# Kernel tuning notes

Hardware: AMD Instinct MI355X
Metric: run time of the kernel (lower is better)

The kernel has to match this reference:

```python
import jax, jax.numpy as jnp
import numpy as np

B, C, H, W = 2, 48, 64, 64
EPS = 1e-5
ROW = [0, 0, 0, H // 4, H // 4, H // 4, H // 2, H // 2, H // 2]
COL = [0, W // 4, W // 2] * 3


def setup_inputs() -> dict:
    key = jax.random.key(0)
    ks = iter(jax.random.split(key, 40))
    s = 1.0 / np.sqrt(C)  # keep unscaled-softmax logits sane
    def rn(shape, scale=1.0):
        return jax.random.normal(next(ks), shape, jnp.float32) * scale
    def ru(shape):
        return jax.random.uniform(next(ks), shape, jnp.float32, 0.5, 1.5)
    return dict(
        input_feature=rn((B, C, H, W)), feat_b=rn((B, C, H, W)),
        feat_c=rn((B, C, H, W)), feat_d=rn((B, C, H, W)),
        W_fa_all=rn((C, C), s), W_fb_all=rn((C, C), s),
        W_fc_all=rn((C, C), s), W_fd_all=rn((C, C), s),
        W_fa=rn((9, C, C), s), W_fb=rn((9, C, C), s),
        W_fc=rn((9, C, C), s), W_fd=rn((9, C, C), s),
        fuse_w=rn((C, 4 * C), s), fuse_b=rn((C,), 0.1),
        fuse_g=ru((C,)), fuse_bb=rn((C,), 0.1), fuse_m=rn((C,), 0.1), fuse_v=ru((C,)),
        fuseP_w=rn((9, C, 4 * C), s), fuseP_b=rn((9, C), 0.1),
        fuseP_g=ru((9, C)), fuseP_bb=rn((9, C), 0.1), fuseP_m=rn((9, C), 0.1), fuseP_v=ru((9, C)),
        gamma_all=rn(()), gamma_p=rn((9,)),
        out_w=rn((C, C, 3, 3), s / 3.0), out_b=rn((C,), 0.1),
        out_g=ru((C,)), out_bb=rn((C,), 0.1), out_m=rn((C,), 0.1), out_v=ru((C,)),
    )


def _attn(q, k, v):
    # q,k,v: [..., C, N] -> energy [..., N, N]; non-standard softmax(max - energy)
    e = jnp.einsum('...cn,...cm->...nm', q, k)
    e = jnp.max(e, axis=-1, keepdims=True) - e
    a = jax.nn.softmax(e, axis=-1)
    return jnp.einsum('...cn,...nm->...cm', v, a)  # torch.matmul(v, attention)


def reference(input_feature, feat_b, feat_c, feat_d,
              W_fa_all, W_fb_all, W_fc_all, W_fd_all,
              W_fa, W_fb, W_fc, W_fd,
              fuse_w, fuse_b, fuse_g, fuse_bb, fuse_m, fuse_v,
              fuseP_w, fuseP_b, fuseP_g, fuseP_bb, fuseP_m, fuseP_v,
              gamma_all, gamma_p,
              out_w, out_b, out_g, out_bb, out_m, out_v):
    h2, w2 = H // 2, W // 2
    N = H * W
    # ---- global branch: channel-wise Linear (bias=False) applied over spatial tokens
    fa = jnp.einsum('dc,bcn->bdn', W_fa_all, input_feature.reshape(B, C, N))
    fb = jnp.einsum('dc,bcn->bdn', W_fb_all, feat_b.reshape(B, C, N))
    fc = jnp.einsum('dc,bcn->bdn', W_fc_all, feat_c.reshape(B, C, N))
    fd = jnp.einsum('dc,bcn->bdn', W_fd_all, feat_d.reshape(B, C, N))
    cat = jnp.concatenate([_attn(fa, fa, fa), _attn(fa, fb, fb),
                           _attn(fa, fc, fc), _attn(fa, fd, fd)], axis=1)
    cat = cat.reshape(B, 4 * C, H, W)
    y = jnp.einsum('oc,bchw->bohw', fuse_w, cat) + fuse_b[None, :, None, None]
    y = (y - fuse_m[:, None, None]) * (fuse_g / jnp.sqrt(fuse_v + EPS))[:, None, None] + fuse_bb[:, None, None]
    atten_all = jax.nn.relu(y)  # Dropout2d is identity at eval
    # ---- 9 overlapping patch branches, vectorized over the patch axis p
    def crops(x):
        return jnp.stack([x[:, :, r:r + h2, c:c + w2] for r, c in zip(ROW, COL)], 0).reshape(9, B, C, h2 * w2)
    pa = jnp.einsum('pdc,pbcn->pbdn', W_fa, crops(input_feature))
    pb = jnp.einsum('pdc,pbcn->pbdn', W_fb, crops(feat_b))
    pc = jnp.einsum('pdc,pbcn->pbdn', W_fc, crops(feat_c))
    pd = jnp.einsum('pdc,pbcn->pbdn', W_fd, crops(feat_d))
    pcat = jnp.concatenate([_attn(pa, pa, pa), _attn(pa, pb, pb),
                            _attn(pa, pc, pc), _attn(pa, pd, pd)], axis=2)
    pcat = pcat.reshape(9, B, 4 * C, h2, w2)
    py = jnp.einsum('poc,pbchw->pbohw', fuseP_w, pcat) + fuseP_b[:, None, :, None, None]
    py = ((py - fuseP_m[:, None, :, None, None])
          * (fuseP_g / jnp.sqrt(fuseP_v + EPS))[:, None, :, None, None]
          + fuseP_bb[:, None, :, None, None])
    patch_out = 0.5 * gamma_p[:, None, None, None, None] * jax.nn.relu(py)
    # ---- combine (overlapping patch regions accumulate additively, as in torch +=)
    out = input_feature + gamma_all * atten_all
    for i, (r, c) in enumerate(zip(ROW, COL)):
        out = out.at[:, :, r:r + h2, c:c + w2].add(patch_out[i])
    # ---- to_out: 3x3 conv + BN(eval) + ReLU
    z = jax.lax.conv_general_dilated(out, out_w, (1, 1), 'SAME',
                                     dimension_numbers=('NCHW', 'OIHW', 'NCHW'))
    z = z + out_b[None, :, None, None]
    z = (z - out_m[:, None, None]) * (out_g / jnp.sqrt(out_v + EPS))[:, None, None] + out_bb[:, None, None]
    return jax.nn.relu(z)
```

## Files before the change

### kernel.cpp

```cpp
#include <hip/hip_runtime.h>
#include <math.h>

typedef _Float16 f16;
typedef f16 f16x8 __attribute__((ext_vector_type(8)));
typedef float f32x4 __attribute__((ext_vector_type(4)));

namespace {
constexpr int B_ = 2, C_ = 48, H_ = 64, W_ = 64;
constexpr int N_ = H_ * W_;
constexpr int NP_ = 1024;
constexpr int C4_ = 4 * C_;
constexpr float EPS_ = 1e-5f;
constexpr float L2E_ = 1.44269504f;
constexpr float REFL2_ = -25.0f * 1.44269504f;
}

#define MFMA32(a, b, c) __builtin_amdgcn_mfma_f32_16x16x32_f16((a), (b), (c), 0, 0, 0)

__device__ inline float fast_exp2(float x) {
#if __has_builtin(__builtin_amdgcn_exp2f)
  return __builtin_amdgcn_exp2f(x);
#else
  float r;
  asm("v_exp_f32 %0, %1" : "=v"(r) : "v"(x));
  return r;
#endif
}

__global__ __launch_bounds__(256) void k_proj_g(
    const float* __restrict__ x0, const float* __restrict__ x1,
    const float* __restrict__ x2, const float* __restrict__ x3,
    const float* __restrict__ w0, const float* __restrict__ w1,
    const float* __restrict__ w2, const float* __restrict__ w3,
    f16* __restrict__ pn, f16* __restrict__ pt) {
  __shared__ float Ws[48 * 48];
  int tid = threadIdx.x;
  int b = blockIdx.y, X = blockIdx.z;
  const float* xp = X == 0 ? x0 : X == 1 ? x1 : X == 2 ? x2 : x3;
  const float* wp = X == 0 ? w0 : X == 1 ? w1 : X == 2 ? w2 : w3;
  for (int i = tid; i < 2304; i += 256) Ws[i] = wp[i];
  __syncthreads();
  int n = blockIdx.x * 256 + tid;
  const float* xb = xp + (size_t)b * 48 * 4096 + n;
  float acc[48];
#pragma unroll
  for (int d = 0; d < 48; ++d) acc[d] = 0.f;
  for (int c0 = 0; c0 < 48; c0 += 4) {
    float xv0 = xb[(size_t)(c0 + 0) * 4096];
    float xv1 = xb[(size_t)(c0 + 1) * 4096];
    float xv2 = xb[(size_t)(c0 + 2) * 4096];
    float xv3 = xb[(size_t)(c0 + 3) * 4096];
#pragma unroll
    for (int d = 0; d < 48; ++d) {
      const float4 wv = *(const float4*)&Ws[d * 48 + c0];
      acc[d] = fmaf(wv.x, xv0, fmaf(wv.y, xv1, fmaf(wv.z, xv2, fmaf(wv.w, xv3, acc[d]))));
    }
  }
  int z2 = X * 2 + b;
  f16* pnb = pn + ((size_t)z2 * 48) * 4096 + n;
#pragma unroll
  for (int d = 0; d < 48; ++d) pnb[(size_t)d * 4096] = (f16)acc[d];
  f16* ptb = pt + ((size_t)z2 * 4096 + n) * 64;
#pragma unroll
  for (int s = 0; s < 6; ++s) {
    f16x8 v;
#pragma unroll
    for (int j = 0; j < 8; ++j) v[j] = (f16)acc[s * 8 + j];
    *(f16x8*)(ptb + s * 8) = v;
  }
  f16x8 zv = {0, 0, 0, 0, 0, 0, 0, 0};
  *(f16x8*)(ptb + 48) = zv;
  *(f16x8*)(ptb + 56) = zv;
}

__global__ __launch_bounds__(256) void k_proj_p(
    const float* __restrict__ x0, const float* __restrict__ x1,
    const float* __restrict__ x2, const float* __restrict__ x3,
    const float* __restrict__ w0, const float* __restrict__ w1,
    const float* __restrict__ w2, const float* __restrict__ w3,
    f16* __restrict__ pn, f16* __restrict__ pt) {
  __shared__ float Ws[48 * 48];
  int tid = threadIdx.x;
  int p = blockIdx.y;
  int X = blockIdx.z >> 1, b = blockIdx.z & 1;
  const float* xp = X == 0 ? x0 : X == 1 ? x1 : X == 2 ? x2 : x3;
  const float* wp = (X == 0 ? w0 : X == 1 ? w1 : X == 2 ? w2 : w3) + (size_t)p * 2304;
  for (int i = tid; i < 2304; i += 256) Ws[i] = wp[i];
  __syncthreads();
  int t = blockIdx.x * 256 + tid;
  int r0 = (p / 3) * 16, c0w = (p % 3) * 16;
  int rr = r0 + (t >> 5), cc = c0w + (t & 31);
  const float* xb = xp + (size_t)b * 48 * 4096 + rr * 64 + cc;
  float acc[48];
#pragma unroll
  for (int d = 0; d < 48; ++d) acc[d] = 0.f;
  for (int c0 = 0; c0 < 48; c0 += 4) {
    float xv0 = xb[(size_t)(c0 + 0) * 4096];
    float xv1 = xb[(size_t)(c0 + 1) * 4096];
    float xv2 = xb[(size_t)(c0 + 2) * 4096];
    float xv3 = xb[(size_t)(c0 + 3) * 4096];
#pragma unroll
    for (int d = 0; d < 48; ++d) {
      const float4 wv = *(const float4*)&Ws[d * 48 + c0];
      acc[d] = fmaf(wv.x, xv0, fmaf(wv.y, xv1, fmaf(wv.z, xv2, fmaf(wv.w, xv3, acc[d]))));
    }
  }
  int z9 = (X * 2 + b) * 9 + p;
  f16* pnb = pn + ((size_t)z9 * 48) * 1024 + t;
#pragma unroll
  for (int d = 0; d < 48; ++d) pnb[(size_t)d * 1024] = (f16)acc[d];
  f16* ptb = pt + ((size_t)z9 * 1024 + t) * 64;
#pragma unroll
  for (int s = 0; s < 6; ++s) {
    f16x8 v;
#pragma unroll
    for (int j = 0; j < 8; ++j) v[j] = (f16)acc[s * 8 + j];
    *(f16x8*)(ptb + s * 8) = v;
  }
  f16x8 zv = {0, 0, 0, 0, 0, 0, 0, 0};
  *(f16x8*)(ptb + 48) = zv;
  *(f16x8*)(ptb + 56) = zv;
}

template <int NT, int NSPLIT, bool PATCH>
__device__ __attribute__((always_inline)) void stats_body(
    const f16* __restrict__ qT_all, const f16* __restrict__ kT_all,
    float* __restrict__ stp, int bx, int by, uint4* Ks) {
  constexpr int MTI = (NT / NSPLIT) / 64;
  int tid = threadIdx.x, wave = tid >> 6, lane = tid & 63, g = lane >> 4, lm = lane & 15;
  int ms = by % NSPLIT, z = by / NSPLIT;
  const f16* qT;
  if (PATCH) {
    int b = (z / 9) % 2, p = z % 9;
    qT = qT_all + ((size_t)(b * 9 + p)) * NT * 64;
  } else {
    int b = z & 1;
    qT = qT_all + (size_t)b * NT * 64;
  }
  const f16* kT = kT_all + (size_t)z * NT * 64;
  int n0 = bx * 128 + wave * 16;
  f16x8 aq0a = *(const f16x8*)(qT + (size_t)(n0 + lm) * 64 + g * 8);
  f16x8 aq1a = *(const f16x8*)(qT + (size_t)(n0 + lm) * 64 + 32 + g * 8);
  f16x8 aq0b = *(const f16x8*)(qT + (size_t)(n0 + 64 + lm) * 64 + g * 8);
  f16x8 aq1b = *(const f16x8*)(qT + (size_t)(n0 + 64 + lm) * 64 + 32 + g * 8);
  const int s0r = tid >> 3, s0c = (tid & 7) * 8;
  const int sw0 = tid ^ ((tid >> 3) & 7);
  const int sw1 = (tid + 256) ^ (((tid + 256) >> 3) & 7);
  const int swl = lm & 7;
  const int c0i = g ^ swl, c1i = (4 + g) ^ swl;
  int t_beg = ms * MTI;
  {
    const f16* src = kT + (size_t)t_beg * 64 * 64;
    Ks[sw0] = *(const uint4*)(src + (size_t)s0r * 64 + s0c);
    Ks[sw1] = *(const uint4*)(src + (size_t)(s0r + 32) * 64 + s0c);
  }
  __syncthreads();
  float zsa[4] = {0.f, 0.f, 0.f, 0.f};
  float zsb[4] = {0.f, 0.f, 0.f, 0.f};
  for (int mt = 0; mt < MTI; ++mt) {
    int cur = mt & 1;
    bool pf = (mt + 1 < MTI);
    uint4 k0v, k1v;
    if (pf) {
      const f16* src = kT + (size_t)(t_beg + mt + 1) * 64 * 64;
      k0v = *(const uint4*)(src + (size_t)s0r * 64 + s0c);
      k1v = *(const uint4*)(src + (size_t)(s0r + 32) * 64 + s0c);
    }
    uint4* kb = Ks + cur * 512;
#pragma unroll
    for (int mf = 0; mf < 4; ++mf) {
      f16x8 b0 = __builtin_bit_cast(f16x8, kb[(16 * mf + lm) * 8 + c0i]);
      f16x8 b1 = __builtin_bit_cast(f16x8, kb[(16 * mf + lm) * 8 + c1i]);
      f32x4 ea = {0.f, 0.f, 0.f, 0.f};
      ea = MFMA32(aq0a, b0, ea);
      ea = MFMA32(aq1a, b1, ea);
      f32x4 eb = {0.f, 0.f, 0.f, 0.f};
      eb = MFMA32(aq0b, b0, eb);
      eb = MFMA32(aq1b, b1, eb);
#pragma unroll
      for (int r = 0; r < 4; ++r) {
        zsa[r] += fast_exp2(fmaf(ea[r], -L2E_, REFL2_));
        zsb[r] += fast_exp2(fmaf(eb[r], -L2E_, REFL2_));
      }
    }
    if (pf) {
      uint4* kn = Ks + (cur ^ 1) * 512;
      kn[sw0] = k0v;
      kn[sw1] = k1v;
    }
    __syncthreads();
  }
#pragma unroll
  for (int mask = 1; mask < 16; mask <<= 1) {
#pragma unroll
    for (int r = 0; r < 4; ++r) {
      zsa[r] += __shfl_xor(zsa[r], mask, 64);
      zsb[r] += __shfl_xor(zsb[r], mask, 64);
    }
  }
  if (lm == 0) {
#pragma unroll
    for (int r = 0; r < 4; ++r) {
      stp[((size_t)z * NT + n0 + 4 * g + r) * NSPLIT + ms] = zsa[r];
      stp[((size_t)z * NT + n0 + 64 + 4 * g + r) * NSPLIT + ms] = zsb[r];
    }
  }
}

__global__ __launch_bounds__(256, 4) void k_stats_all(
    const f16* __restrict__ pg_t, float* __restrict__ stpg,
    const f16* __restrict__ pp_t, float* __restrict__ stpp) {
  __shared__ uint4 Ks[2 * 512];
  int bid = blockIdx.x;
  if (bid < 1024) {
    stats_body<N_, 4, false>(pg_t, pg_t, stpg, bid & 31, bid >> 5, Ks);
  } else {
    int pid = bid - 1024;
    stats_body<NP_, 1, true>(pp_t, pp_t, stpp, pid & 7, pid >> 3, Ks);
  }
}

__global__ __launch_bounds__(256) void k_merge_all(
    const float* __restrict__ stpg, float* __restrict__ stg,
    const float* __restrict__ stpp, float* __restrict__ stp2) {
  int i = blockIdx.x * 256 + threadIdx.x;
  if (i < 8 * N_) {
    const float* p = stpg + (size_t)i * 4;
    float Z = p[0] + p[1] + p[2] + p[3];
    stg[i] = REFL2_ - __log2f(Z);
  } else {
    int j = i - 8 * N_;
    if (j < 72 * NP_) stp2[j] = REFL2_ - __log2f(stpp[j]);
  }
}

template <int NT, int NSPLIT, bool PATCH>
__device__ __attribute__((always_inline)) void pv_body(
    const f16* __restrict__ qT_all, const f16* __restrict__ kT_all,
    const f16* __restrict__ vN_all, const float* __restrict__ st_all,
    float* __restrict__ out_all, int bx, int by,
    float* As2, uint4* Qs, uint4* Vs, uint2* wt2) {
  constexpr int CH = NT / NSPLIT;
  constexpr int NTI = CH / 64;
  int tid = threadIdx.x, wave = tid >> 6, lane = tid & 63, g = lane >> 4, lm = lane & 15;
  int ns = by % NSPLIT, z = by / NSPLIT;
  const f16 *qT, *kT, *vN;
  float* op;
  if (PATCH) {
    int X = z / 18, b = (z / 9) % 2, p = z % 9;
    qT = qT_all + ((size_t)(b * 9 + p)) * NT * 64;
    op = out_all + ((size_t)((p * 2 + b) * C4_ + X * 48)) * NT;
  } else {
    int X = z >> 1, b = z & 1;
    qT = qT_all + (size_t)b * NT * 64;
    op = out_all + ((size_t)(b * C4_ + X * 48)) * NT;
  }
  kT = kT_all + (size_t)z * NT * 64;
  vN = vN_all + (size_t)z * 48 * NT;
  const float* st = st_all + (size_t)z * NT + ns * CH;
  ((float4*)As2)[tid] = ((const float4*)st)[tid];
  int mwa = bx * 128 + wave * 16;
  int mwb = mwa + 64;
  f16x8 bk0a = *(const f16x8*)(kT + (size_t)(mwa + lm) * 64 + g * 8);
  f16x8 bk1a = *(const f16x8*)(kT + (size_t)(mwa + lm) * 64 + 32 + g * 8);
  f16x8 bk0b = *(const f16x8*)(kT + (size_t)(mwb + lm) * 64 + g * 8);
  f16x8 bk1b = *(const f16x8*)(kT + (size_t)(mwb + lm) * 64 + 32 + g * 8);
  const int s0r = tid >> 3, s0c = (tid & 7) * 8;
  const int sw0 = tid ^ ((tid >> 3) & 7);
  const int sw1 = (tid + 256) ^ (((tid + 256) >> 3) & 7);
  const int swl = lm & 7;
  const int c0i = g ^ swl, c1i = (4 + g) ^ swl;
  int t_beg = ns * NTI;
  {
    const f16* qsrc = qT + (size_t)t_beg * 64 * 64;
    Qs[sw0] = *(const uint4*)(qsrc + (size_t)s0r * 64 + s0c);
    Qs[sw1] = *(const uint4*)(qsrc + (size_t)(s0r + 32) * 64 + s0c);
    Vs[sw0] = *(const uint4*)(vN + (size_t)s0r * NT + t_beg * 64 + s0c);
    if (tid < 128)
      Vs[sw1] = *(const uint4*)(vN + (size_t)(s0r + 32) * NT + t_beg * 64 + s0c);
  }
  __syncthreads();
  f32x4 oa0 = {0.f, 0.f, 0.f, 0.f}, oa1 = {0.f, 0.f, 0.f, 0.f}, oa2 = {0.f, 0.f, 0.f, 0.f};
  f32x4 ob0 = {0.f, 0.f, 0.f, 0.f}, ob1 = {0.f, 0.f, 0.f, 0.f}, ob2 = {0.f, 0.f, 0.f, 0.f};
  int wbufa = wave * 512;
  int wbufb = wave * 512 + 256;
  int rba = wbufa + lm * 16;
  int rbb = wbufb + lm * 16;
  for (int nt = 0; nt < NTI; ++nt) {
    bool pf = (nt + 1 < NTI);
    uint4 q0v, q1v, v0v, v1v;
    if (pf) {
      int tn = t_beg + nt + 1;
      const f16* qsrc = qT + (size_t)tn * 64 * 64;
      q0v = *(const uint4*)(qsrc + (size_t)s0r * 64 + s0c);
      q1v = *(const uint4*)(qsrc + (size_t)(s0r + 32) * 64 + s0c);
      v0v = *(const uint4*)(vN + (size_t)s0r * NT + tn * 64 + s0c);
      if (tid < 128)
        v1v = *(const uint4*)(vN + (size_t)(s0r + 32) * NT + tn * 64 + s0c);
    }
    f32x4 ea[4], eb[4];
#pragma unroll
    for (int nf = 0; nf < 4; ++nf) {
      f16x8 a0 = __builtin_bit_cast(f16x8, Qs[(16 * nf + lm) * 8 + c0i]);
      f16x8 a1 = __builtin_bit_cast(f16x8, Qs[(16 * nf + lm) * 8 + c1i]);
      f32x4 ta = {0.f, 0.f, 0.f, 0.f};
      ta = MFMA32(a0, bk0a, ta);
      ta = MFMA32(a1, bk1a, ta);
      ea[nf] = ta;
      f32x4 tb = {0.f, 0.f, 0.f, 0.f};
      tb = MFMA32(a0, bk0b, tb);
      tb = MFMA32(a1, bk1b, tb);
      eb[nf] = tb;
    }
#pragma unroll
    for (int nf = 0; nf < 4; ++nf) {
      float4 a4 = *(const float4*)&As2[nt * 64 + nf * 16 + g * 4];
      float wa0 = fast_exp2(fmaf(ea[nf][0], -L2E_, a4.x));
      float wa1 = fast_exp2(fmaf(ea[nf][1], -L2E_, a4.y));
      float wa2 = fast_exp2(fmaf(ea[nf][2], -L2E_, a4.z));
      float wa3 = fast_exp2(fmaf(ea[nf][3], -L2E_, a4.w));
      float wb0 = fast_exp2(fmaf(eb[nf][0], -L2E_, a4.x));
      float wb1 = fast_exp2(fmaf(eb[nf][1], -L2E_, a4.y));
      float wb2 = fast_exp2(fmaf(eb[nf][2], -L2E_, a4.z));
      float wb3 = fast_exp2(fmaf(eb[nf][3], -L2E_, a4.w));
      unsigned la = __builtin_bit_cast(unsigned, __builtin_amdgcn_cvt_pkrtz(wa0, wa1));
      unsigned ha = __builtin_bit_cast(unsigned, __builtin_amdgcn_cvt_pkrtz(wa2, wa3));
      unsigned lb = __builtin_bit_cast(unsigned, __builtin_amdgcn_cvt_pkrtz(wb0, wb1));
      unsigned hb = __builtin_bit_cast(unsigned, __builtin_amdgcn_cvt_pkrtz(wb2, wb3));
      int s = 2 * nf + (g >> 1);
      int so = ((s ^ swl) * 2) + (g & 1);
      wt2[wbufa + lm * 16 + so] = make_uint2(la, ha);
      wt2[wbufb + lm * 16 + so] = make_uint2(lb, hb);
    }
    __builtin_amdgcn_sched_barrier(0);
    f16x8 bw0a = __builtin_bit_cast(f16x8, *(const uint4*)&wt2[rba + c0i * 2]);
    f16x8 bw1a = __builtin_bit_cast(f16x8, *(const uint4*)&wt2[rba + c1i * 2]);
    f16x8 bw0b = __builtin_bit_cast(f16x8, *(const uint4*)&wt2[rbb + c0i * 2]);
    f16x8 bw1b = __builtin_bit_cast(f16x8, *(const uint4*)&wt2[rbb + c1i * 2]);
#pragma unroll
    for (int cf = 0; cf < 3; ++cf) {
      f16x8 av0 = __builtin_bit_cast(f16x8, Vs[(16 * cf + lm) * 8 + c0i]);
      f16x8 av1 = __builtin_bit_cast(f16x8, Vs[(16 * cf + lm) * 8 + c1i]);
      if (cf == 0) {
        oa0 = MFMA32(av0, bw0a, oa0); oa0 = MFMA32(av1, bw1a, oa0);
        ob0 = MFMA32(av0, bw0b, ob0); ob0 = MFMA32(av1, bw1b, ob0);
      }
      if (cf == 1) {
        oa1 = MFMA32(av0, bw0a, oa1); oa1 = MFMA32(av1, bw1a, oa1);
        ob1 = MFMA32(av0, bw0b, ob1); ob1 = MFMA32(av1, bw1b, ob1);
      }
      if (cf == 2) {
        oa2 = MFMA32(av0, bw0a, oa2); oa2 = MFMA32(av1, bw1a, oa2);
        ob2 = MFMA32(av0, bw0b, ob2); ob2 = MFMA32(av1, bw1b, ob2);
      }
    }
    __syncthreads();
    if (pf) {
      Qs[sw0] = q0v;
      Qs[sw1] = q1v;
      Vs[sw0] = v0v;
      if (tid < 128) Vs[sw1] = v1v;
    }
    __syncthreads();
  }
  if (NSPLIT == 1) {
#pragma unroll
    for (int r = 0; r < 4; ++r) {
      op[(size_t)(0 + 4 * g + r) * NT + mwa + lm] = oa0[r];
      op[(size_t)(16 + 4 * g + r) * NT + mwa + lm] = oa1[r];
      op[(size_t)(32 + 4 * g + r) * NT + mwa + lm] = oa2[r];
      op[(size_t)(0 + 4 * g + r) * NT + mwb + lm] = ob0[r];
      op[(size_t)(16 + 4 * g + r) * NT + mwb + lm] = ob1[r];
      op[(size_t)(32 + 4 * g + r) * NT + mwb + lm] = ob2[r];
    }
  } else {
#pragma unroll
    for (int r = 0; r < 4; ++r) {
      atomicAdd(&op[(size_t)(0 + 4 * g + r) * NT + mwa + lm], oa0[r]);
      atomicAdd(&op[(size_t)(16 + 4 * g + r) * NT + mwa + lm], oa1[r]);
      atomicAdd(&op[(size_t)(32 + 4 * g + r) * NT + mwa + lm], oa2[r]);
      atomicAdd(&op[(size_t)(0 + 4 * g + r) * NT + mwb + lm], ob0[r]);
      atomicAdd(&op[(size_t)(16 + 4 * g + r) * NT + mwb + lm], ob1[r]);
      atomicAdd(&op[(size_t)(32 + 4 * g + r) * NT + mwb + lm], ob2[r]);
    }
  }
}

__global__ __launch_bounds__(256, 4) void k_pv_all(
    const f16* __restrict__ pg_t, const f16* __restrict__ pg_n,
    const float* __restrict__ statsg, float* __restrict__ cat,
    const f16* __restrict__ pp_t, const f16* __restrict__ pp_n,
    const float* __restrict__ statsp, float* __restrict__ pcat) {
  __shared__ float As2[1024];
  __shared__ uint4 Qs[512];
  __shared__ uint4 Vs[384];
  __shared__ uint2 wt2[2048];
  int bid = blockIdx.x;
  if (bid < 1024) {
    pv_body<N_, 4, false>(pg_t, pg_t, pg_n, statsg, cat, bid & 31, bid >> 5,
                          As2, Qs, Vs, wt2);
  } else {
    int pid = bid - 1024;
    pv_body<NP_, 1, true>(pp_t, pp_t, pp_n, statsp, pcat, pid & 7, pid >> 3,
                          As2, Qs, Vs, wt2);
  }
}

__global__ __launch_bounds__(256) void k_fuse_global(
    const float* __restrict__ cat, const float* __restrict__ fw,
    const float* __restrict__ fb, const float* __restrict__ fg,
    const float* __restrict__ fbb, const float* __restrict__ fm,
    const float* __restrict__ fv, const float* __restrict__ gamma_all,
    const float* __restrict__ input, float* __restrict__ comb) {
  int idx = blockIdx.x * 256 + threadIdx.x;
  int n4 = idx & 1023;
  int rest = idx >> 10;
  int o = rest % C_;
  int b = rest / C_;
  const float* cr = cat + (size_t)b * C4_ * N_ + n4 * 4;
  const float* wr = fw + (size_t)o * C4_;
  float4 acc = {0.f, 0.f, 0.f, 0.f};
#pragma unroll 8
  for (int c = 0; c < C4_; ++c) {
    float4 xv = *(const float4*)(cr + (size_t)c * N_);
    float w = wr[c];
    acc.x = fmaf(w, xv.x, acc.x); acc.y = fmaf(w, xv.y, acc.y);
    acc.z = fmaf(w, xv.z, acc.z); acc.w = fmaf(w, xv.w, acc.w);
  }
  float scale = fg[o] * rsqrtf(fv[o] + EPS_);
  float sh = fb[o] - fm[o], bb = fbb[o], ga = gamma_all[0];
  float4 inv = *(const float4*)(input + ((size_t)(b * C_ + o) * N_) + n4 * 4);
  float4 out;
  out.x = inv.x + ga * fmaxf((acc.x + sh) * scale + bb, 0.f);
  out.y = inv.y + ga * fmaxf((acc.y + sh) * scale + bb, 0.f);
  out.z = inv.z + ga * fmaxf((acc.z + sh) * scale + bb, 0.f);
  out.w = inv.w + ga * fmaxf((acc.w + sh) * scale + bb, 0.f);
  *(float4*)(comb + ((size_t)(b * C_ + o) * N_) + n4 * 4) = out;
}

__global__ __launch_bounds__(256) void k_fuse_patch(
    const float* __restrict__ pcat, const float* __restrict__ fw,
    const float* __restrict__ fb, const float* __restrict__ fg,
    const float* __restrict__ fbb, const float* __restrict__ fm,
    const float* __restrict__ fv, const float* __restrict__ gamma_p,
    float* __restrict__ py) {
  int idx = blockIdx.x * 256 + threadIdx.x;
  int t4 = idx & 255;
  int rest = idx >> 8;
  int o = rest % C_; rest /= C_;
  int b = rest % B_;
  int p = rest / B_;
  const float* cr = pcat + ((size_t)(p * B_ + b) * C4_) * NP_ + t4 * 4;
  const float* wr = fw + (size_t)(p * C_ + o) * C4_;
  float4 acc = {0.f, 0.f, 0.f, 0.f};
#pragma unroll 8
  for (int c = 0; c < C4_; ++c) {
    float4 xv = *(const float4*)(cr + (size_t)c * NP_);
    float w = wr[c];
    acc.x = fmaf(w, xv.x, acc.x); acc.y = fmaf(w, xv.y, acc.y);
    acc.z = fmaf(w, xv.z, acc.z); acc.w = fmaf(w, xv.w, acc.w);
  }
  int po = p * C_ + o;
  float scale = fg[po] * rsqrtf(fv[po] + EPS_);
  float sh = fb[po] - fm[po], bb = fbb[po], gp = 0.5f * gamma_p[p];
  float4 out;
  out.x = gp * fmaxf((acc.x + sh) * scale + bb, 0.f);
  out.y = gp * fmaxf((acc.y + sh) * scale + bb, 0.f);
  out.z = gp * fmaxf((acc.z + sh) * scale + bb, 0.f);
  out.w = gp * fmaxf((acc.w + sh) * scale + bb, 0.f);
  *(float4*)(py + ((size_t)(p * B_ + b) * C_ + o) * NP_ + t4 * 4) = out;
}

__global__ __launch_bounds__(256) void k_combine(
    const float* __restrict__ py, const float* __restrict__ comb,
    f16* __restrict__ combh) {
  int idx = blockIdx.x * 256 + threadIdx.x;
  int w = idx & (W_ - 1);
  int h = (idx >> 6) & (H_ - 1);
  int rest = idx >> 12;
  int ch = rest % C_;
  int b = rest / C_;
  float val = comb[idx];
#pragma unroll
  for (int p = 0; p < 9; ++p) {
    int r0 = (p / 3) * 16, c0 = (p % 3) * 16;
    if (h >= r0 && h < r0 + 32 && w >= c0 && w < c0 + 32)
      val += py[((size_t)(p * B_ + b) * C_ + ch) * NP_ + (h - r0) * 32 + (w - c0)];
  }
  combh[idx] = (f16)val;
}

__global__ __launch_bounds__(256) void k_conv2(
    const f16* __restrict__ combh, const float* __restrict__ cw,
    const float* __restrict__ cb, const float* __restrict__ cg,
    const float* __restrict__ cbb, const float* __restrict__ cm,
    const float* __restrict__ cv, float* __restrict__ out) {
  __shared__ uint4 inh[2304];
  int tid = threadIdx.x;
  int h0 = blockIdx.x * 4, ocg = blockIdx.y, b = blockIdx.z;
  for (int i = tid; i < 2304; i += 256) {
    int c = i / 48;
    int rem = i - c * 48;
    int r = rem >> 3, u = rem & 7;
    int hh = h0 - 1 + r;
    uint4 val = make_uint4(0, 0, 0, 0);
    if (hh >= 0 && hh < H_)
      val = *(const uint4*)(combh + (((size_t)(b * C_ + c) * H_ + hh) * W_ + u * 8));
    inh[i] = val;
  }
  __syncthreads();
  int w = tid & 63, dh = tid >> 6;
  float acc[6] = {0.f, 0.f, 0.f, 0.f, 0.f, 0.f};
  const f16* lds = (const f16*)inh;
  int wm = w > 0 ? w - 1 : 0;
  int wp = w < 63 ? w + 1 : 63;
  for (int c = 0; c < 48; ++c) {
    float v[9];
#pragma unroll
    for (int r = 0; r < 3; ++r) {
      const f16* row = lds + (size_t)(c * 6 + dh + r) * 64;
      float lf = (float)row[wm];
      float md = (float)row[w];
      float rt = (float)row[wp];
      v[r * 3 + 0] = (w > 0) ? lf : 0.f;
      v[r * 3 + 1] = md;
      v[r * 3 + 2] = (w < 63) ? rt : 0.f;
    }
#pragma unroll
    for (int j = 0; j < 6; ++j) {
      const float* wr = cw + (size_t)((ocg * 6 + j) * 48 + c) * 9;
#pragma unroll
      for (int k = 0; k < 9; ++k) acc[j] = fmaf(v[k], wr[k], acc[j]);
    }
  }
#pragma unroll
  for (int j = 0; j < 6; ++j) {
    int o = ocg * 6 + j;
    float scale = cg[o] * rsqrtf(cv[o] + EPS_);
    float y = (acc[j] + cb[o] - cm[o]) * scale + cbb[o];
    out[(size_t)(b * C_ + o) * N_ + (h0 + dh) * 64 + w] = fmaxf(y, 0.f);
  }
}

extern "C" void kernel_launch(void* const* d_in, const int* in_sizes, int n_in,
                              void* d_out, int out_size, void* d_ws, size_t ws_size,
                              hipStream_t stream) {
  (void)in_sizes; (void)n_in; (void)out_size; (void)ws_size;
  const float* x[4];
  const float* Wall[4];
  const float* Wp[4];
  for (int i = 0; i < 4; ++i) {
    x[i] = (const float*)d_in[i];
    Wall[i] = (const float*)d_in[4 + i];
    Wp[i] = (const float*)d_in[8 + i];
  }
  const float* fuse_w = (const float*)d_in[12];
  const float* fuse_b = (const float*)d_in[13];
  const float* fuse_g = (const float*)d_in[14];
  const float* fuse_bb = (const float*)d_in[15];
  const float* fuse_m = (const float*)d_in[16];
  const float* fuse_v = (const float*)d_in[17];
  const float* fuseP_w = (const float*)d_in[18];
  const float* fuseP_b = (const float*)d_in[19];
  const float* fuseP_g = (const float*)d_in[20];
  const float* fuseP_bb = (const float*)d_in[21];
  const float* fuseP_m = (const float*)d_in[22];
  const float* fuseP_v = (const float*)d_in[23];
  const float* gamma_all = (const float*)d_in[24];
  const float* gamma_p = (const float*)d_in[25];
  const float* out_w = (const float*)d_in[26];
  const float* out_b = (const float*)d_in[27];
  const float* out_g = (const float*)d_in[28];
  const float* out_bb = (const float*)d_in[29];
  const float* out_m = (const float*)d_in[30];
  const float* out_v = (const float*)d_in[31];

  char* base = (char*)d_ws;
  size_t off = 0;
  auto carve = [&](size_t bytes) {
    char* p = base + off;
    off += (bytes + 255) & ~(size_t)255;
    return p;
  };
  f16* projg_n = (f16*)carve((size_t)8 * 48 * N_ * 2);
  f16* projg_t = (f16*)carve((size_t)8 * N_ * 64 * 2);
  f16* projp_n = (f16*)carve((size_t)72 * 48 * NP_ * 2);
  f16* projp_t = (f16*)carve((size_t)72 * NP_ * 64 * 2);
  float* stpg = (float*)carve((size_t)8 * N_ * 4 * 4);
  float* stpp = (float*)carve((size_t)72 * NP_ * 4);
  float* statsg = (float*)carve((size_t)8 * N_ * 4);
  float* statsp = (float*)carve((size_t)72 * NP_ * 4);
  float* cat = (float*)carve((size_t)B_ * C4_ * N_ * 4);
  float* pcat = (float*)carve((size_t)9 * B_ * C4_ * NP_ * 4);
  float* comb = (float*)carve((size_t)B_ * C_ * N_ * 4);
  float* py = (float*)carve((size_t)9 * B_ * C_ * NP_ * 4);
  f16* combh = (f16*)carve((size_t)B_ * C_ * N_ * 2);

  dim3 blk(256);

  k_proj_g<<<dim3(16, 2, 4), blk, 0, stream>>>(
      x[0], x[1], x[2], x[3], Wall[0], Wall[1], Wall[2], Wall[3], projg_n, projg_t);
  k_proj_p<<<dim3(4, 9, 8), blk, 0, stream>>>(
      x[0], x[1], x[2], x[3], Wp[0], Wp[1], Wp[2], Wp[3], projp_n, projp_t);

  k_stats_all<<<dim3(1600), blk, 0, stream>>>(projg_t, stpg, projp_t, stpp);
  k_merge_all<<<dim3((8 * N_ + 72 * NP_ + 255) / 256), blk, 0, stream>>>(
      stpg, statsg, stpp, statsp);

  (void)hipMemsetAsync(cat, 0, (size_t)B_ * C4_ * N_ * sizeof(float), stream);
  k_pv_all<<<dim3(1600), blk, 0, stream>>>(
      projg_t, projg_n, statsg, cat, projp_t, projp_n, statsp, pcat);

  k_fuse_global<<<(B_ * C_ * (N_ / 4)) / 256, blk, 0, stream>>>(
      cat, fuse_w, fuse_b, fuse_g, fuse_bb, fuse_m, fuse_v, gamma_all, x[0], comb);
  k_fuse_patch<<<(9 * B_ * C_ * (NP_ / 4)) / 256, blk, 0, stream>>>(
      pcat, fuseP_w, fuseP_b, fuseP_g, fuseP_bb, fuseP_m, fuseP_v, gamma_p, py);
  k_combine<<<(B_ * C_ * N_) / 256, blk, 0, stream>>>(py, comb, combh);
  k_conv2<<<dim3(16, 8, 2), blk, 0, stream>>>(
      combh, out_w, out_b, out_g, out_bb, out_m, out_v, (float*)d_out);
}
```

Baseline: 262.0 us.

## Merge projection and fuse kernels, drop LDS stats staging, raise stats occupancy

Merges the global and patch projection kernels into one launch, and likewise the global and patch fuse kernels, so fewer kernels launch and the small grids share the GPU. The PV kernel now reads the softmax stats straight from global memory instead of staging them in shared memory, which saves LDS and a store. The stats kernel's launch-bounds occupancy hint goes from 4 to 6 blocks. The memset is moved earlier in the stream. Risks are more register pressure in the stats kernel and extra global loads for the stats reads.

```diff
diff --git a/kernel.cpp b/kernel.cpp
--- a/kernel.cpp
+++ b/kernel.cpp
@@ -27,21 +27,9 @@
 #endif
 }
 
-__global__ __launch_bounds__(256) void k_proj_g(
-    const float* __restrict__ x0, const float* __restrict__ x1,
-    const float* __restrict__ x2, const float* __restrict__ x3,
-    const float* __restrict__ w0, const float* __restrict__ w1,
-    const float* __restrict__ w2, const float* __restrict__ w3,
-    f16* __restrict__ pn, f16* __restrict__ pt) {
-  __shared__ float Ws[48 * 48];
-  int tid = threadIdx.x;
-  int b = blockIdx.y, X = blockIdx.z;
-  const float* xp = X == 0 ? x0 : X == 1 ? x1 : X == 2 ? x2 : x3;
-  const float* wp = X == 0 ? w0 : X == 1 ? w1 : X == 2 ? w2 : w3;
-  for (int i = tid; i < 2304; i += 256) Ws[i] = wp[i];
-  __syncthreads();
-  int n = blockIdx.x * 256 + tid;
-  const float* xb = xp + (size_t)b * 48 * 4096 + n;
+__device__ __attribute__((always_inline)) void proj_body(
+    const float* __restrict__ xb, const float* __restrict__ Ws,
+    f16* __restrict__ pnb, size_t pn_stride, f16* __restrict__ ptb) {
   float acc[48];
 #pragma unroll
   for (int d = 0; d < 48; ++d) acc[d] = 0.f;
@@ -56,11 +44,8 @@
       acc[d] = fmaf(wv.x, xv0, fmaf(wv.y, xv1, fmaf(wv.z, xv2, fmaf(wv.w, xv3, acc[d]))));
     }
   }
-  int z2 = X * 2 + b;
-  f16* pnb = pn + ((size_t)z2 * 48) * 4096 + n;
-#pragma unroll
-  for (int d = 0; d < 48; ++d) pnb[(size_t)d * 4096] = (f16)acc[d];
-  f16* ptb = pt + ((size_t)z2 * 4096 + n) * 64;
+#pragma unroll
+  for (int d = 0; d < 48; ++d) pnb[(size_t)d * pn_stride] = (f16)acc[d];
 #pragma unroll
   for (int s = 0; s < 6; ++s) {
     f16x8 v;
@@ -73,53 +58,48 @@
   *(f16x8*)(ptb + 56) = zv;
 }
 
-__global__ __launch_bounds__(256) void k_proj_p(
+__global__ __launch_bounds__(256) void k_proj_all(
     const float* __restrict__ x0, const float* __restrict__ x1,
     const float* __restrict__ x2, const float* __restrict__ x3,
     const float* __restrict__ w0, const float* __restrict__ w1,
     const float* __restrict__ w2, const float* __restrict__ w3,
-    f16* __restrict__ pn, f16* __restrict__ pt) {
+    const float* __restrict__ wp0, const float* __restrict__ wp1,
+    const float* __restrict__ wp2, const float* __restrict__ wp3,
+    f16* __restrict__ pgn, f16* __restrict__ pgt,
+    f16* __restrict__ ppn, f16* __restrict__ ppt) {
   __shared__ float Ws[48 * 48];
   int tid = threadIdx.x;
-  int p = blockIdx.y;
-  int X = blockIdx.z >> 1, b = blockIdx.z & 1;
-  const float* xp = X == 0 ? x0 : X == 1 ? x1 : X == 2 ? x2 : x3;
-  const float* wp = (X == 0 ? w0 : X == 1 ? w1 : X == 2 ? w2 : w3) + (size_t)p * 2304;
-  for (int i = tid; i < 2304; i += 256) Ws[i] = wp[i];
-  __syncthreads();
-  int t = blockIdx.x * 256 + tid;
-  int r0 = (p / 3) * 16, c0w = (p % 3) * 16;
-  int rr = r0 + (t >> 5), cc = c0w + (t & 31);
-  const float* xb = xp + (size_t)b * 48 * 4096 + rr * 64 + cc;
-  float acc[48];
-#pragma unroll
-  for (int d = 0; d < 48; ++d) acc[d] = 0.f;
-  for (int c0 = 0; c0 < 48; c0 += 4) {
-    float xv0 = xb[(size_t)(c0 + 0) * 4096];
-    float xv1 = xb[(size_t)(c0 + 1) * 4096];
-    float xv2 = xb[(size_t)(c0 + 2) * 4096];
-    float xv3 = xb[(size_t)(c0 + 3) * 4096];
-#pragma unroll
-    for (int d = 0; d < 48; ++d) {
-      const float4 wv = *(const float4*)&Ws[d * 48 + c0];
-      acc[d] = fmaf(wv.x, xv0, fmaf(wv.y, xv1, fmaf(wv.z, xv2, fmaf(wv.w, xv3, acc[d]))));
-    }
-  }
-  int z9 = (X * 2 + b) * 9 + p;
-  f16* pnb = pn + ((size_t)z9 * 48) * 1024 + t;
-#pragma unroll
-  for (int d = 0; d < 48; ++d) pnb[(size_t)d * 1024] = (f16)acc[d];
-  f16* ptb = pt + ((size_t)z9 * 1024 + t) * 64;
-#pragma unroll
-  for (int s = 0; s < 6; ++s) {
-    f16x8 v;
-#pragma unroll
-    for (int j = 0; j < 8; ++j) v[j] = (f16)acc[s * 8 + j];
-    *(f16x8*)(ptb + s * 8) = v;
-  }
-  f16x8 zv = {0, 0, 0, 0, 0, 0, 0, 0};
-  *(f16x8*)(ptb + 48) = zv;
-  *(f16x8*)(ptb + 56) = zv;
+  int bid = blockIdx.x;
+  if (bid < 128) {
+    int bx = bid & 15, b = (bid >> 4) & 1, X = bid >> 5;
+    const float* xp = X == 0 ? x0 : X == 1 ? x1 : X == 2 ? x2 : x3;
+    const float* wp = X == 0 ? w0 : X == 1 ? w1 : X == 2 ? w2 : w3;
+    for (int i = tid; i < 2304; i += 256) Ws[i] = wp[i];
+    __syncthreads();
+    int n = bx * 256 + tid;
+    int z2 = X * 2 + b;
+    proj_body(xp + (size_t)b * 48 * 4096 + n, Ws,
+              pgn + ((size_t)z2 * 48) * 4096 + n, 4096,
+              pgt + ((size_t)z2 * 4096 + n) * 64);
+  } else {
+    int pid = bid - 128;
+    int bx = pid & 3;
+    int rest = pid >> 2;
+    int p = rest % 9;
+    int zb = rest / 9;
+    int X = zb >> 1, b = zb & 1;
+    const float* xp = X == 0 ? x0 : X == 1 ? x1 : X == 2 ? x2 : x3;
+    const float* wp = (X == 0 ? wp0 : X == 1 ? wp1 : X == 2 ? wp2 : wp3) + (size_t)p * 2304;
+    for (int i = tid; i < 2304; i += 256) Ws[i] = wp[i];
+    __syncthreads();
+    int t = bx * 256 + tid;
+    int r0 = (p / 3) * 16, c0w = (p % 3) * 16;
+    int rr = r0 + (t >> 5), cc = c0w + (t & 31);
+    int z9 = (X * 2 + b) * 9 + p;
+    proj_body(xp + (size_t)b * 48 * 4096 + rr * 64 + cc, Ws,
+              ppn + ((size_t)z9 * 48) * 1024 + t, 1024,
+              ppt + ((size_t)z9 * 1024 + t) * 64);
+  }
 }
 
 template <int NT, int NSPLIT, bool PATCH>
@@ -207,7 +187,7 @@
   }
 }
 
-__global__ __launch_bounds__(256, 4) void k_stats_all(
+__global__ __launch_bounds__(256, 6) void k_stats_all(
     const f16* __restrict__ pg_t, float* __restrict__ stpg,
     const f16* __restrict__ pp_t, float* __restrict__ stpp) {
   __shared__ uint4 Ks[2 * 512];
@@ -239,7 +219,7 @@
     const f16* __restrict__ qT_all, const f16* __restrict__ kT_all,
     const f16* __restrict__ vN_all, const float* __restrict__ st_all,
     float* __restrict__ out_all, int bx, int by,
-    float* As2, uint4* Qs, uint4* Vs, uint2* wt2) {
+    uint4* Qs, uint4* Vs, uint2* wt2) {
   constexpr int CH = NT / NSPLIT;
   constexpr int NTI = CH / 64;
   int tid = threadIdx.x, wave = tid >> 6, lane = tid & 63, g = lane >> 4, lm = lane & 15;
@@ -258,7 +238,6 @@
   kT = kT_all + (size_t)z * NT * 64;
   vN = vN_all + (size_t)z * 48 * NT;
   const float* st = st_all + (size_t)z * NT + ns * CH;
-  ((float4*)As2)[tid] = ((const float4*)st)[tid];
   int mwa = bx * 128 + wave * 16;
   int mwb = mwa + 64;
   f16x8 bk0a = *(const f16x8*)(kT + (size_t)(mwa + lm) * 64 + g * 8);
@@ -314,7 +293,7 @@
     }
 #pragma unroll
     for (int nf = 0; nf < 4; ++nf) {
-      float4 a4 = *(const float4*)&As2[nt * 64 + nf * 16 + g * 4];
+      float4 a4 = *(const float4*)(st + nt * 64 + nf * 16 + g * 4);
       float wa0 = fast_exp2(fmaf(ea[nf][0], -L2E_, a4.x));
       float wa1 = fast_exp2(fmaf(ea[nf][1], -L2E_, a4.y));
       float wa2 = fast_exp2(fmaf(ea[nf][2], -L2E_, a4.z));
@@ -391,84 +370,84 @@
     const float* __restrict__ statsg, float* __restrict__ cat,
     const f16* __restrict__ pp_t, const f16* __restrict__ pp_n,
     const float* __restrict__ statsp, float* __restrict__ pcat) {
-  __shared__ float As2[1024];
   __shared__ uint4 Qs[512];
   __shared__ uint4 Vs[384];
   __shared__ uint2 wt2[2048];
   int bid = blockIdx.x;
   if (bid < 1024) {
     pv_body<N_, 4, false>(pg_t, pg_t, pg_n, statsg, cat, bid & 31, bid >> 5,
-                          As2, Qs, Vs, wt2);
+                          Qs, Vs, wt2);
   } else {
     int pid = bid - 1024;
     pv_body<NP_, 1, true>(pp_t, pp_t, pp_n, statsp, pcat, pid & 7, pid >> 3,
-                          As2, Qs, Vs, wt2);
-  }
-}
-
-__global__ __launch_bounds__(256) void k_fuse_global(
+                          Qs, Vs, wt2);
+  }
+}
+
+__global__ __launch_bounds__(256) void k_fuse_all(
     const float* __restrict__ cat, const float* __restrict__ fw,
     const float* __restrict__ fb, const float* __restrict__ fg,
     const float* __restrict__ fbb, const float* __restrict__ fm,
     const float* __restrict__ fv, const float* __restrict__ gamma_all,
-    const float* __restrict__ input, float* __restrict__ comb) {
-  int idx = blockIdx.x * 256 + threadIdx.x;
-  int n4 = idx & 1023;
-  int rest = idx >> 10;
-  int o = rest % C_;
-  int b = rest / C_;
-  const float* cr = cat + (size_t)b * C4_ * N_ + n4 * 4;
-  const float* wr = fw + (size_t)o * C4_;
-  float4 acc = {0.f, 0.f, 0.f, 0.f};
+    const float* __restrict__ input, float* __restrict__ comb,
+    const float* __restrict__ pcat, const float* __restrict__ pfw,
+    const float* __restrict__ pfb, const float* __restrict__ pfg,
+    const float* __restrict__ pfbb, const float* __restrict__ pfm,
+    const float* __restrict__ pfv, const float* __restrict__ gamma_p,
+    float* __restrict__ py) {
+  int bid = blockIdx.x;
+  if (bid < 384) {
+    int idx = bid * 256 + threadIdx.x;
+    int n4 = idx & 1023;
+    int rest = idx >> 10;
+    int o = rest % C_;
+    int b = rest / C_;
+    const float* cr = cat + (size_t)b * C4_ * N_ + n4 * 4;
+    const float* wr = fw + (size_t)o * C4_;
+    float4 acc = {0.f, 0.f, 0.f, 0.f};
 #pragma unroll 8
-  for (int c = 0; c < C4_; ++c) {
-    float4 xv = *(const float4*)(cr + (size_t)c * N_);
-    float w = wr[c];
-    acc.x = fmaf(w, xv.x, acc.x); acc.y = fmaf(w, xv.y, acc.y);
-    acc.z = fmaf(w, xv.z, acc.z); acc.w = fmaf(w, xv.w, acc.w);
-  }
-  float scale = fg[o] * rsqrtf(fv[o] + EPS_);
-  float sh = fb[o] - fm[o], bb = fbb[o], ga = gamma_all[0];
-  float4 inv = *(const float4*)(input + ((size_t)(b * C_ + o) * N_) + n4 * 4);
-  float4 out;
-  out.x = inv.x + ga * fmaxf((acc.x + sh) * scale + bb, 0.f);
-  out.y = inv.y + ga * fmaxf((acc.y + sh) * scale + bb, 0.f);
-  out.z = inv.z + ga * fmaxf((acc.z + sh) * scale + bb, 0.f);
-  out.w = inv.w + ga * fmaxf((acc.w + sh) * scale + bb, 0.f);
-  *(float4*)(comb + ((size_t)(b * C_ + o) * N_) + n4 * 4) = out;
-}
-
-__global__ __launch_bounds__(256) void k_fuse_patch(
-    const float* __restrict__ pcat, const float* __restrict__ fw,
-    const float* __restrict__ fb, const float* __restrict__ fg,
-    const float* __restrict__ fbb, const float* __restrict__ fm,
-    const float* __restrict__ fv, const float* __restrict__ gamma_p,
-    float* __restrict__ py) {
-  int idx = blockIdx.x * 256 + threadIdx.x;
-  int t4 = idx & 255;
-  int rest = idx >> 8;
-  int o = rest % C_; rest /= C_;
-  int b = rest % B_;
-  int p = rest / B_;
-  const float* cr = pcat + ((size_t)(p * B_ + b) * C4_) * NP_ + t4 * 4;
-  const float* wr = fw + (size_t)(p * C_ + o) * C4_;
-  float4 acc = {0.f, 0.f, 0.f, 0.f};
+    for (int c = 0; c < C4_; ++c) {
+      float4 xv = *(const float4*)(cr + (size_t)c * N_);
+      float w = wr[c];
+      acc.x = fmaf(w, xv.x, acc.x); acc.y = fmaf(w, xv.y, acc.y);
+      acc.z = fmaf(w, xv.z, acc.z); acc.w = fmaf(w, xv.w, acc.w);
+    }
+    float scale = fg[o] * rsqrtf(fv[o] + EPS_);
+    float sh = fb[o] - fm[o], bb = fbb[o], ga = gamma_all[0];
+    float4 inv = *(const float4*)(input + ((size_t)(b * C_ + o) * N_) + n4 * 4);
+    float4 out;
+    out.x = inv.x + ga * fmaxf((acc.x + sh) * scale + bb, 0.f);
+    out.y = inv.y + ga * fmaxf((acc.y + sh) * scale + bb, 0.f);
+    out.z = inv.z + ga * fmaxf((acc.z + sh) * scale + bb, 0.f);
+    out.w = inv.w + ga * fmaxf((acc.w + sh) * scale + bb, 0.f);
+    *(float4*)(comb + ((size_t)(b * C_ + o) * N_) + n4 * 4) = out;
+  } else {
+    int idx = (bid - 384) * 256 + threadIdx.x;
+    int t4 = idx & 255;
+    int rest = idx >> 8;
+    int o = rest % C_; rest /= C_;
+    int b = rest % B_;
+    int p = rest / B_;
+    const float* cr = pcat + ((size_t)(p * B_ + b) * C4_) * NP_ + t4 * 4;
+    const float* wr = pfw + (size_t)(p * C_ + o) * C4_;
+    float4 acc = {0.f, 0.f, 0.f, 0.f};
 #pragma unroll 8
-  for (int c = 0; c < C4_; ++c) {
-    float4 xv = *(const float4*)(cr + (size_t)c * NP_);
-    float w = wr[c];
-    acc.x = fmaf(w, xv.x, acc.x); acc.y = fmaf(w, xv.y, acc.y);
-    acc.z = fmaf(w, xv.z, acc.z); acc.w = fmaf(w, xv.w, acc.w);
-  }
-  int po = p * C_ + o;
-  float scale = fg[po] * rsqrtf(fv[po] + EPS_);
-  float sh = fb[po] - fm[po], bb = fbb[po], gp = 0.5f * gamma_p[p];
-  float4 out;
-  out.x = gp * fmaxf((acc.x + sh) * scale + bb, 0.f);
-  out.y = gp * fmaxf((acc.y + sh) * scale + bb, 0.f);
-  out.z = gp * fmaxf((acc.z + sh) * scale + bb, 0.f);
-  out.w = gp * fmaxf((acc.w + sh) * scale + bb, 0.f);
-  *(float4*)(py + ((size_t)(p * B_ + b) * C_ + o) * NP_ + t4 * 4) = out;
+    for (int c = 0; c < C4_; ++c) {
+      float4 xv = *(const float4*)(cr + (size_t)c * NP_);
+      float w = wr[c];
+      acc.x = fmaf(w, xv.x, acc.x); acc.y = fmaf(w, xv.y, acc.y);
+      acc.z = fmaf(w, xv.z, acc.z); acc.w = fmaf(w, xv.w, acc.w);
+    }
+    int po = p * C_ + o;
+    float scale = pfg[po] * rsqrtf(pfv[po] + EPS_);
+    float sh = pfb[po] - pfm[po], bb = pfbb[po], gp = 0.5f * gamma_p[p];
+    float4 out;
+    out.x = gp * fmaxf((acc.x + sh) * scale + bb, 0.f);
+    out.y = gp * fmaxf((acc.y + sh) * scale + bb, 0.f);
+    out.z = gp * fmaxf((acc.z + sh) * scale + bb, 0.f);
+    out.w = gp * fmaxf((acc.w + sh) * scale + bb, 0.f);
+    *(float4*)(py + ((size_t)(p * B_ + b) * C_ + o) * NP_ + t4 * 4) = out;
+  }
 }
 
 __global__ __launch_bounds__(256) void k_combine(
@@ -598,22 +577,20 @@
 
   dim3 blk(256);
 
-  k_proj_g<<<dim3(16, 2, 4), blk, 0, stream>>>(
-      x[0], x[1], x[2], x[3], Wall[0], Wall[1], Wall[2], Wall[3], projg_n, projg_t);
-  k_proj_p<<<dim3(4, 9, 8), blk, 0, stream>>>(
-      x[0], x[1], x[2], x[3], Wp[0], Wp[1], Wp[2], Wp[3], projp_n, projp_t);
+  (void)hipMemsetAsync(cat, 0, (size_t)B_ * C4_ * N_ * sizeof(float), stream);
+  k_proj_all<<<dim3(416), blk, 0, stream>>>(
+      x[0], x[1], x[2], x[3], Wall[0], Wall[1], Wall[2], Wall[3],
+      Wp[0], Wp[1], Wp[2], Wp[3], projg_n, projg_t, projp_n, projp_t);
 
   k_stats_all<<<dim3(1600), blk, 0, stream>>>(projg_t, stpg, projp_t, stpp);
   k_merge_all<<<dim3((8 * N_ + 72 * NP_ + 255) / 256), blk, 0, stream>>>(
       stpg, statsg, stpp, statsp);
 
-  (void)hipMemsetAsync(cat, 0, (size_t)B_ * C4_ * N_ * sizeof(float), stream);
   k_pv_all<<<dim3(1600), blk, 0, stream>>>(
       projg_t, projg_n, statsg, cat, projp_t, projp_n, statsp, pcat);
 
-  k_fuse_global<<<(B_ * C_ * (N_ / 4)) / 256, blk, 0, stream>>>(
-      cat, fuse_w, fuse_b, fuse_g, fuse_bb, fuse_m, fuse_v, gamma_all, x[0], comb);
-  k_fuse_patch<<<(9 * B_ * C_ * (NP_ / 4)) / 256, blk, 0, stream>>>(
+  k_fuse_all<<<dim3(1248), blk, 0, stream>>>(
+      cat, fuse_w, fuse_b, fuse_g, fuse_bb, fuse_m, fuse_v, gamma_all, x[0], comb,
       pcat, fuseP_w, fuseP_b, fuseP_g, fuseP_bb, fuseP_m, fuseP_v, gamma_p, py);
   k_combine<<<(B_ * C_ * N_) / 256, blk, 0, stream>>>(py, comb, combh);
   k_conv2<<<dim3(16, 8, 2), blk, 0, stream>>>(
```

Result: faster. 251.6 us (-4.0%).
